# Optimization experiments

Hardware: AMD Instinct MI355X
Metric: run time of the kernel (lower is better)

Reference implementation:

```python
import jax, jax.numpy as jnp
import numpy as np

WS = 7
SHIFT = 3
NH = 16
DIM = 512
MLP = 2048
EMB = 512
EPS = 1e-6


def _rel_pos_index(ws):
    coords = np.stack(np.meshgrid(np.arange(ws), np.arange(ws), indexing='ij'))  # [2,ws,ws]
    flat = coords.reshape(2, -1)
    rel = flat[:, :, None] - flat[:, None, :]          # [2,N,N]
    rel = rel.transpose(1, 2, 0).copy()                # [N,N,2]
    rel[..., 0] += ws - 1
    rel[..., 1] += ws - 1
    rel[..., 0] *= 2 * ws - 1
    return rel.sum(-1)                                 # [N,N] int


def _shift_mask(H, W, ws, shift):
    img = np.zeros((H, W))
    cnt = 0
    for hs in (slice(0, -ws), slice(-ws, -shift), slice(-shift, None)):
        for wsl in (slice(0, -ws), slice(-ws, -shift), slice(-shift, None)):
            img[hs, wsl] = cnt
            cnt += 1
    win = img.reshape(H // ws, ws, W // ws, ws).transpose(0, 2, 1, 3).reshape(-1, ws * ws)
    diff = win[:, None, :] - win[:, :, None]           # [nW,N,N]
    return np.where(diff != 0, -100.0, 0.0).astype(np.float32)


def setup_inputs() -> dict:
    key = jax.random.key(0)
    ks = jax.random.split(key, 16)
    B, H, W = 16, 56, 56
    C, mlp, emb_dim = DIM, MLP, EMB
    std = 0.02
    inp = {
        'x': jax.random.normal(ks[0], (B, H * W, C), jnp.float32),
        'emb': jax.random.normal(ks[1], (B, emb_dim), jnp.float32),
        'adaLN_w': jax.random.normal(ks[2], (emb_dim, 6 * C), jnp.float32) * std,
        'adaLN_b': jnp.zeros((6 * C,), jnp.float32),
        'qkv_w': jax.random.normal(ks[3], (C, 3 * C), jnp.float32) * std,
        'qkv_b': jnp.zeros((3 * C,), jnp.float32),
        'proj_w': jax.random.normal(ks[4], (C, C), jnp.float32) * std,
        'proj_b': jnp.zeros((C,), jnp.float32),
        'rel_bias_table': jax.random.normal(ks[5], ((2 * WS - 1) ** 2, NH), jnp.float32) * std,
        'ff_w1': jax.random.normal(ks[6], (C, mlp), jnp.float32) * std,
        'ff_b1': jnp.zeros((mlp,), jnp.float32),
        'ff_w2': jax.random.normal(ks[7], (mlp, C), jnp.float32) * std,
        'ff_b2': jnp.zeros((C,), jnp.float32),
        'H': H,
        'W': W,
    }
    return inp


def _ln(t):
    mu = t.mean(-1, keepdims=True)
    var = ((t - mu) ** 2).mean(-1, keepdims=True)
    return (t - mu) / jnp.sqrt(var + EPS)


def reference(x, emb, adaLN_w, adaLN_b, qkv_w, qkv_b, proj_w, proj_b,
              rel_bias_table, ff_w1, ff_b1, ff_w2, ff_b2, H, W):
    B, L, C = x.shape
    dh = C // NH
    scale = dh ** (-0.5)
    N = WS * WS
    nWh, nWw = H // WS, W // WS
    nW = nWh * nWw

    # AdaLN modulation
    mod = jax.nn.silu(emb) @ adaLN_w + adaLN_b
    sh_sa, sc_sa, g_sa, sh_ff, sc_ff, g_ff = jnp.split(mod, 6, axis=-1)

    h = _ln(x) * (1.0 + sc_sa[:, None, :]) + sh_sa[:, None, :]
    h = h.reshape(B, H, W, C)
    h = jnp.roll(h, (-SHIFT, -SHIFT), axis=(1, 2))

    # window partition -> [B*nW, N, C]
    win = h.reshape(B, nWh, WS, nWw, WS, C).transpose(0, 1, 3, 2, 4, 5).reshape(B * nW, N, C)

    qkv = (win @ qkv_w + qkv_b).reshape(B * nW, N, 3, NH, dh).transpose(2, 0, 3, 1, 4)
    q, k, v = qkv[0], qkv[1], qkv[2]                   # [B_, NH, N, dh]
    attn = jnp.einsum('bhnd,bhmd->bhnm', q, k) * scale

    idx = _rel_pos_index(WS)
    bias = rel_bias_table[idx.reshape(-1)].reshape(N, N, NH).transpose(2, 0, 1)
    attn = attn + bias[None]

    mask = jnp.asarray(_shift_mask(H, W, WS, SHIFT))   # [nW,N,N]
    attn = attn.reshape(B, nW, NH, N, N) + mask[None, :, None]
    attn = jax.nn.softmax(attn.reshape(B * nW, NH, N, N), axis=-1)

    out = jnp.einsum('bhnm,bhmd->bnhd', attn, v).reshape(B * nW, N, C)
    out = out @ proj_w + proj_b

    # window reverse + unshift
    h = out.reshape(B, nWh, nWw, WS, WS, C).transpose(0, 1, 3, 2, 4, 5).reshape(B, H, W, C)
    h = jnp.roll(h, (SHIFT, SHIFT), axis=(1, 2)).reshape(B, L, C)

    x = x + g_sa[:, None, :] * h

    h = _ln(x) * (1.0 + sc_ff[:, None, :]) + sh_ff[:, None, :]
    ffo = jax.nn.gelu(h @ ff_w1 + ff_b1, approximate=False) @ ff_w2 + ff_b2
    return x + g_ff[:, None, :] * ffo
```

## Files before the change

kernel.cpp:

```cpp
#include <hip/hip_runtime.h>
#include <cmath>

typedef unsigned short u16;
typedef unsigned short u16x2 __attribute__((ext_vector_type(2)));
typedef unsigned short u16x4 __attribute__((ext_vector_type(4)));
typedef unsigned short u16x8 __attribute__((ext_vector_type(8)));
typedef short s16x8 __attribute__((ext_vector_type(8)));
typedef float f32x4 __attribute__((ext_vector_type(4)));
typedef float f32x2 __attribute__((ext_vector_type(2)));

#define B_SZ 16
#define HW 56
#define L_TOK 3136
#define C_DIM 512
#define NHEAD 16
#define DHEAD 32
#define WS7 7
#define NWIN 49
#define ROWS_TOTAL 50176
#define MLP_DIM 2048

__device__ __forceinline__ float bf2f(u16 u) {
    union { unsigned int i; float f; } z;
    z.i = ((unsigned int)u) << 16;
    return z.f;
}
__device__ __forceinline__ u16 f2bf(float f) {
    union { float f; unsigned int i; } z;
    z.f = f;
    unsigned int r = z.i + 0x7fffu + ((z.i >> 16) & 1u);
    return (u16)(r >> 16);
}

__device__ __forceinline__ void gl_lds16(const u16* g, u16* l) {
    __builtin_amdgcn_global_load_lds(
        (const __attribute__((address_space(1))) unsigned int*)g,
        (__attribute__((address_space(3))) unsigned int*)l,
        16, 0, 0);
}

__global__ __launch_bounds__(256)
void mod_kernel(const float* __restrict__ emb, const float* __restrict__ w,
                const float* __restrict__ bias, float* __restrict__ mod)
{
    int b = blockIdx.y;
    int o = blockIdx.x * 256 + threadIdx.x;
    __shared__ float se[512];
    for (int i = threadIdx.x; i < 512; i += 256) {
        float e = emb[b * 512 + i];
        se[i] = e / (1.0f + expf(-e));
    }
    __syncthreads();
    float acc = bias[o];
    #pragma unroll 8
    for (int k = 0; k < 512; ++k)
        acc += se[k] * w[(size_t)k * 3072 + o];
    mod[b * 3072 + o] = acc;
}

__global__ __launch_bounds__(1024)
void transpose_kernel(const float* __restrict__ W, u16* __restrict__ Wt, int K, int N)
{
    __shared__ float tile[32][33];
    int k0 = blockIdx.x * 32, n0 = blockIdx.y * 32;
    tile[threadIdx.y][threadIdx.x] = W[(size_t)(k0 + threadIdx.y) * N + (n0 + threadIdx.x)];
    __syncthreads();
    Wt[(size_t)(n0 + threadIdx.y) * K + (k0 + threadIdx.x)] = f2bf(tile[threadIdx.x][threadIdx.y]);
}

template<int WINDOWED>
__global__ __launch_bounds__(256)
void ln_kernel(const float* __restrict__ xin, const float* __restrict__ mod,
               u16* __restrict__ out, int shOff, int scOff, int rowBase)
{
    int wv   = threadIdx.x >> 6;
    int lane = threadIdx.x & 63;
    int rbl = blockIdx.x * 4 + wv;
    int rb  = rbl + rowBase;
    int b = rb / L_TOK, l = rb - b * L_TOK;
    const float* xr = xin + (size_t)rb * C_DIM;
    int c0 = lane * 8;
    f32x4 u0 = *(const f32x4*)(xr + c0);
    f32x4 u1 = *(const f32x4*)(xr + c0 + 4);
    float s = u0.x + u0.y + u0.z + u0.w + u1.x + u1.y + u1.z + u1.w;
    float q = u0.x*u0.x + u0.y*u0.y + u0.z*u0.z + u0.w*u0.w
            + u1.x*u1.x + u1.y*u1.y + u1.z*u1.z + u1.w*u1.w;
    #pragma unroll
    for (int off = 32; off > 0; off >>= 1) {
        s += __shfl_xor(s, off);
        q += __shfl_xor(q, off);
    }
    float mu = s * (1.0f / 512.0f);
    float var = q * (1.0f / 512.0f) - mu * mu;
    float rstd = rsqrtf(var + 1e-6f);
    const float* mb = mod + b * 3072;
    f32x4 sc0 = *(const f32x4*)(mb + scOff + c0);
    f32x4 sc1 = *(const f32x4*)(mb + scOff + c0 + 4);
    f32x4 sh0 = *(const f32x4*)(mb + shOff + c0);
    f32x4 sh1 = *(const f32x4*)(mb + shOff + c0 + 4);
    float y[8];
    y[0] = (u0.x - mu) * rstd * (1.0f + sc0.x) + sh0.x;
    y[1] = (u0.y - mu) * rstd * (1.0f + sc0.y) + sh0.y;
    y[2] = (u0.z - mu) * rstd * (1.0f + sc0.z) + sh0.z;
    y[3] = (u0.w - mu) * rstd * (1.0f + sc0.w) + sh0.w;
    y[4] = (u1.x - mu) * rstd * (1.0f + sc1.x) + sh1.x;
    y[5] = (u1.y - mu) * rstd * (1.0f + sc1.y) + sh1.y;
    y[6] = (u1.z - mu) * rstd * (1.0f + sc1.z) + sh1.z;
    y[7] = (u1.w - mu) * rstd * (1.0f + sc1.w) + sh1.w;
    size_t drow;
    if (WINDOWED) {
        int hh = l / HW, ww = l - hh * HW;
        int hs = hh - 3; if (hs < 0) hs += HW;
        int ws2 = ww - 3; if (ws2 < 0) ws2 += HW;
        int wi = (hs / WS7) * 8 + (ws2 / WS7);
        int n  = (hs % WS7) * WS7 + (ws2 % WS7);
        int b_local = rbl / L_TOK;
        drow = (size_t)((b_local * 64 + wi) * NWIN + n);
    } else {
        drow = (size_t)rbl;
    }
    u16x8 o;
    #pragma unroll
    for (int i = 0; i < 8; ++i) o[i] = f2bf(y[i]);
    *(u16x8*)(out + drow * C_DIM + c0) = o;
}

template<int EPI>
__global__ __launch_bounds__(256)
void gemm128(const u16* __restrict__ A, const u16* __restrict__ Bt,
             const float* __restrict__ bias, void* __restrict__ outv,
             const float* __restrict__ resid, const float* __restrict__ mod,
             int N, int K, int rowOffset)
{
    __shared__ u16 sA[128][32];
    __shared__ u16 sB[128][32];
    const int tid  = threadIdx.x;
    const int lane = tid & 63;
    const int wave = tid >> 6;
    const int wr = (wave >> 1) * 64;
    const int wc = (wave & 1) * 64;
    const int quad = lane >> 4;
    const int mrow = lane & 15;
    const int rowBase = blockIdx.x * 128;
    const int colBase = blockIdx.y * 128;

    const int r0   = wave * 32;
    const int lrow = lane >> 2;
    const int lcol = (lane & 3) * 8;
    const u16* gA = A  + (size_t)(rowBase + r0 + lrow) * K + lcol;
    const u16* gB = Bt + (size_t)(colBase + r0 + lrow) * K + lcol;
    u16* lA0 = &sA[r0][0];
    u16* lA1 = &sA[r0 + 16][0];
    u16* lB0 = &sB[r0][0];
    u16* lB1 = &sB[r0 + 16][0];
    const size_t gstep = (size_t)16 * K;

    f32x4 acc[4][4] = {};

    for (int kk = 0; kk < K; kk += 32) {
        __syncthreads();
        gl_lds16(gA + kk,         lA0);
        gl_lds16(gA + kk + gstep, lA1);
        gl_lds16(gB + kk,         lB0);
        gl_lds16(gB + kk + gstep, lB1);
        __syncthreads();
        s16x8 af[4], bg[4];
        #pragma unroll
        for (int tt = 0; tt < 4; ++tt) {
            af[tt] = *(const s16x8*)&sA[wr + tt * 16 + mrow][quad * 8];
            bg[tt] = *(const s16x8*)&sB[wc + tt * 16 + mrow][quad * 8];
        }
        #pragma unroll
        for (int tm = 0; tm < 4; ++tm)
            #pragma unroll
            for (int tn = 0; tn < 4; ++tn)
                acc[tm][tn] = __builtin_amdgcn_mfma_f32_16x16x32_bf16(
                    af[tm], bg[tn], acc[tm][tn], 0, 0, 0);
    }

    #pragma unroll
    for (int tm = 0; tm < 4; ++tm) {
        #pragma unroll
        for (int tn = 0; tn < 4; ++tn) {
            int col = colBase + wc + tn * 16 + mrow;
            float bv = bias[col];
            #pragma unroll
            for (int i = 0; i < 4; ++i) {
                int r = rowBase + wr + tm * 16 + quad * 4 + i;
                float v = acc[tm][tn][i] + bv;
                if constexpr (EPI == 0) {
                    ((u16*)outv)[(size_t)r * N + col] = f2bf(v);
                } else if constexpr (EPI == 1) {
                    float g = 0.5f * v * (1.0f + erff(v * 0.70710678118654752f));
                    ((u16*)outv)[(size_t)r * N + col] = f2bf(g);
                } else if constexpr (EPI == 2) {
                    int rg = r + rowOffset;
                    int b = rg / L_TOK;
                    int rem = rg - b * L_TOK;
                    int wi = rem / NWIN;
                    int n  = rem - wi * NWIN;
                    int hs  = (wi >> 3) * WS7 + n / WS7;
                    int ws2 = (wi & 7) * WS7 + n % WS7;
                    int hh = hs + 3;  if (hh >= HW)  hh -= HW;
                    int ww = ws2 + 3; if (ww >= HW)  ww -= HW;
                    size_t dst = ((size_t)(b * L_TOK + hh * HW + ww)) * C_DIM + col;
                    float g = mod[b * 3072 + 1024 + col];
                    ((float*)outv)[dst] = resid[dst] + g * v;
                } else {
                    int rg = r + rowOffset;
                    int b = rg / L_TOK;
                    size_t dst = (size_t)rg * C_DIM + col;
                    float g = mod[b * 3072 + 2560 + col];
                    ((float*)outv)[dst] = resid[dst] + g * v;
                }
            }
        }
    }
}

__global__ __launch_bounds__(256)
void attn_mfma(const u16* __restrict__ qkv, const float* __restrict__ bias_table,
               u16* __restrict__ out)
{
    const int w    = blockIdx.x;
    const int hg   = blockIdx.y;
    const int wave = threadIdx.x >> 6;
    const int lane = threadIdx.x & 63;
    const int h    = hg * 4 + wave;
    const int wi   = w & 63;
    const int quad = lane >> 4;
    const int mrow = lane & 15;

    __shared__ u16 sP[4][64][72];
    __shared__ u16 sVt[4][32][72];
    __shared__ float sBias[4][169];

    const u16* qb = qkv + (size_t)w * NWIN * 1536 + h * DHEAD;

    for (int e = lane; e < 169; e += 64)
        sBias[wave][e] = bias_table[e * NHEAD + h];

    #pragma unroll
    for (int rr = 0; rr < 4; ++rr) {
        int e = rr * 64 + lane;
        int r = e >> 2, d0 = (e & 3) * 8;
        u16x8 vv = {};
        if (e < 196)
            vv = *(const u16x8*)(qb + (size_t)r * 1536 + 1024 + d0);
        #pragma unroll
        for (int j = 0; j < 8; ++j)
            sVt[wave][d0 + j][r] = vv[j];
    }

    s16x8 qf[4], kf[4];
    #pragma unroll
    for (int t = 0; t < 4; ++t) {
        int r = t * 16 + mrow; if (r > 48) r = 48;
        qf[t] = *(const s16x8*)(qb + (size_t)r * 1536 + quad * 8);
        kf[t] = *(const s16x8*)(qb + (size_t)r * 1536 + 512 + quad * 8);
    }
    __syncthreads();

    f32x4 sacc[4][4] = {};
    #pragma unroll
    for (int tm = 0; tm < 4; ++tm)
        #pragma unroll
        for (int tn = 0; tn < 4; ++tn)
            sacc[tm][tn] = __builtin_amdgcn_mfma_f32_16x16x32_bf16(
                qf[tm], kf[tn], sacc[tm][tn], 0, 0, 0);

    const float scale = 0.17677669529663687f;
    const int wh = wi >> 3, ww = wi & 7;

    int khA[4], kwA[4], rkA[4], nOK[4];
    #pragma unroll
    for (int tn = 0; tn < 4; ++tn) {
        int n = tn * 16 + mrow;
        nOK[tn] = (n < NWIN);
        int nc = n > 48 ? 48 : n;
        khA[tn] = nc / 7; kwA[tn] = nc - khA[tn] * 7;
        int gkh = wh * 7 + khA[tn], gkw = ww * 7 + kwA[tn];
        rkA[tn] = (gkh < 49 ? 0 : (gkh < 53 ? 1 : 2)) * 3
                + (gkw < 49 ? 0 : (gkw < 53 ? 1 : 2));
    }

    #pragma unroll
    for (int tm = 0; tm < 4; ++tm) {
        #pragma unroll
        for (int i = 0; i < 4; ++i) {
            int m = tm * 16 + quad * 4 + i;
            int mc = m > 48 ? 48 : m;
            int qh = mc / 7, qw = mc - qh * 7;
            int gqh = wh * 7 + qh, gqw = ww * 7 + qw;
            int rq = (gqh < 49 ? 0 : (gqh < 53 ? 1 : 2)) * 3
                   + (gqw < 49 ? 0 : (gqw < 53 ? 1 : 2));
            float v[4];
            #pragma unroll
            for (int tn = 0; tn < 4; ++tn) {
                float s = sacc[tm][tn][i] * scale;
                s += sBias[wave][(qh - khA[tn] + 6) * 13 + (qw - kwA[tn] + 6)];
                if (rq != rkA[tn]) s -= 100.0f;
                v[tn] = nOK[tn] ? s : -1e30f;
            }
            float mx = fmaxf(fmaxf(v[0], v[1]), fmaxf(v[2], v[3]));
            mx = fmaxf(mx, __shfl_xor(mx, 1));
            mx = fmaxf(mx, __shfl_xor(mx, 2));
            mx = fmaxf(mx, __shfl_xor(mx, 4));
            mx = fmaxf(mx, __shfl_xor(mx, 8));
            float p0 = __expf(v[0] - mx), p1 = __expf(v[1] - mx);
            float p2 = __expf(v[2] - mx), p3 = __expf(v[3] - mx);
            float sum = p0 + p1 + p2 + p3;
            sum += __shfl_xor(sum, 1);
            sum += __shfl_xor(sum, 2);
            sum += __shfl_xor(sum, 4);
            sum += __shfl_xor(sum, 8);
            float inv = 1.0f / sum;
            float pp[4] = { p0 * inv, p1 * inv, p2 * inv, p3 * inv };
            #pragma unroll
            for (int tn = 0; tn < 4; ++tn) {
                float po = __shfl_xor(pp[tn], 1);
                if (!(mrow & 1)) {
                    unsigned int pk = (unsigned int)f2bf(pp[tn])
                                    | ((unsigned int)f2bf(po) << 16);
                    *(unsigned int*)&sP[wave][m][tn * 16 + mrow] = pk;
                }
            }
        }
    }
    __syncthreads();

    f32x4 oacc[2][4] = {};
    #pragma unroll
    for (int ks = 0; ks < 2; ++ks) {
        s16x8 vf[2], pf[4];
        #pragma unroll
        for (int td = 0; td < 2; ++td)
            vf[td] = *(const s16x8*)&sVt[wave][td * 16 + mrow][ks * 32 + quad * 8];
        #pragma unroll
        for (int tm = 0; tm < 4; ++tm)
            pf[tm] = *(const s16x8*)&sP[wave][tm * 16 + mrow][ks * 32 + quad * 8];
        #pragma unroll
        for (int td = 0; td < 2; ++td)
            #pragma unroll
            for (int tm = 0; tm < 4; ++tm)
                oacc[td][tm] = __builtin_amdgcn_mfma_f32_16x16x32_bf16(
                    vf[td], pf[tm], oacc[td][tm], 0, 0, 0);
    }

    #pragma unroll
    for (int tm = 0; tm < 4; ++tm) {
        int m = tm * 16 + mrow;
        if (m < NWIN) {
            u16* orow = out + ((size_t)(w * NWIN + m)) * C_DIM + h * DHEAD;
            #pragma unroll
            for (int td = 0; td < 2; ++td) {
                u16x4 ov;
                #pragma unroll
                for (int i = 0; i < 4; ++i) ov[i] = f2bf(oacc[td][tm][i]);
                *(u16x4*)(orow + td * 16 + quad * 4) = ov;
            }
        }
    }
}

extern "C" void kernel_launch(void* const* d_in, const int* in_sizes, int n_in,
                              void* d_out, int out_size, void* d_ws, size_t ws_size,
                              hipStream_t stream)
{
    const float* x       = (const float*)d_in[0];
    const float* emb     = (const float*)d_in[1];
    const float* adaLN_w = (const float*)d_in[2];
    const float* adaLN_b = (const float*)d_in[3];
    const float* qkv_w   = (const float*)d_in[4];
    const float* qkv_b   = (const float*)d_in[5];
    const float* proj_w  = (const float*)d_in[6];
    const float* proj_b  = (const float*)d_in[7];
    const float* relb    = (const float*)d_in[8];
    const float* ff_w1   = (const float*)d_in[9];
    const float* ff_b1   = (const float*)d_in[10];
    const float* ff_w2   = (const float*)d_in[11];
    const float* ff_b2   = (const float*)d_in[12];
    float* outp = (float*)d_out;

    char* ws = (char*)d_ws;
    float* mod   = (float*)(ws + 0);
    u16* wT_qkv  = (u16*)(ws + 196608);
    u16* wT_proj = (u16*)(ws + 1769472);
    u16* wT_ff1  = (u16*)(ws + 2293760);
    u16* wT_ff2  = (u16*)(ws + 4390912);
    char* slots  = ws + 6488064;

    const size_t perB_S = (size_t)L_TOK * C_DIM * sizeof(u16);
    const size_t perB_L = (size_t)L_TOK * MLP_DIM * sizeof(u16);

    int CB = 4;
    if (ws_size >= 6488064 + 8 * (perB_S + perB_L)) CB = 8;

    const int nChunks   = B_SZ / CB;
    const int chunkRows = CB * L_TOK;
    u16* slotS = (u16*)slots;
    u16* slotL = (u16*)(slots + (size_t)CB * perB_S);

    mod_kernel<<<dim3(12, 16), dim3(256), 0, stream>>>(emb, adaLN_w, adaLN_b, mod);
    transpose_kernel<<<dim3(16, 48), dim3(32, 32), 0, stream>>>(qkv_w,  wT_qkv, 512, 1536);
    transpose_kernel<<<dim3(16, 16), dim3(32, 32), 0, stream>>>(proj_w, wT_proj, 512, 512);
    transpose_kernel<<<dim3(16, 64), dim3(32, 32), 0, stream>>>(ff_w1,  wT_ff1, 512, 2048);
    transpose_kernel<<<dim3(64, 16), dim3(32, 32), 0, stream>>>(ff_w2,  wT_ff2, 2048, 512);

    for (int c = 0; c < nChunks; ++c) {
        int row0 = c * chunkRows;
        ln_kernel<1><<<dim3(chunkRows / 4), dim3(256), 0, stream>>>(
            x, mod, slotS, 0, 512, row0);
        gemm128<0><<<dim3(chunkRows / 128, 12), dim3(256), 0, stream>>>(
            slotS, wT_qkv, qkv_b, slotL, nullptr, mod, 1536, 512, 0);
        attn_mfma<<<dim3(CB * 64, 4), dim3(256), 0, stream>>>(slotL, relb, slotS);
        gemm128<2><<<dim3(chunkRows / 128, 4), dim3(256), 0, stream>>>(
            slotS, wT_proj, proj_b, outp, x, mod, 512, 512, row0);
        ln_kernel<0><<<dim3(chunkRows / 4), dim3(256), 0, stream>>>(
            outp, mod, slotS, 1536, 2048, row0);
        gemm128<1><<<dim3(chunkRows / 128, 16), dim3(256), 0, stream>>>(
            slotS, wT_ff1, ff_b1, slotL, nullptr, mod, 2048, 512, 0);
        gemm128<3><<<dim3(chunkRows / 128, 4), dim3(256), 0, stream>>>(
            slotL, wT_ff2, ff_b2, outp, outp, mod, 512, 2048, row0);
    }
}
```

Measured before the change: 1.091 ms.

## Triple-buffer LDS tiles in gemm128 to overlap global loads with MFMA

The GEMM main loop now keeps three LDS stages and issues the global-to-LDS copy for tile t+2 while tile t is computed. Explicit vmcnt waits and a single barrier per iteration replace the two syncthreads around each load. The goal is to hide global memory latency behind MFMA work. In exchange, LDS use per block triples, which can lower occupancy, and correctness depends on the hand-written waitcnt counts.

```diff
diff --git a/kernel.cpp b/kernel.cpp
--- a/kernel.cpp
+++ b/kernel.cpp
@@ -132,8 +132,8 @@
              const float* __restrict__ resid, const float* __restrict__ mod,
              int N, int K, int rowOffset)
 {
-    __shared__ u16 sA[128][32];
-    __shared__ u16 sB[128][32];
+    __shared__ u16 sA[3][128][32];
+    __shared__ u16 sB[3][128][32];
     const int tid  = threadIdx.x;
     const int lane = tid & 63;
     const int wave = tid >> 6;
@@ -149,26 +149,31 @@
     const int lcol = (lane & 3) * 8;
     const u16* gA = A  + (size_t)(rowBase + r0 + lrow) * K + lcol;
     const u16* gB = Bt + (size_t)(colBase + r0 + lrow) * K + lcol;
-    u16* lA0 = &sA[r0][0];
-    u16* lA1 = &sA[r0 + 16][0];
-    u16* lB0 = &sB[r0][0];
-    u16* lB1 = &sB[r0 + 16][0];
     const size_t gstep = (size_t)16 * K;
 
     f32x4 acc[4][4] = {};
-
-    for (int kk = 0; kk < K; kk += 32) {
-        __syncthreads();
-        gl_lds16(gA + kk,         lA0);
-        gl_lds16(gA + kk + gstep, lA1);
-        gl_lds16(gB + kk,         lB0);
-        gl_lds16(gB + kk + gstep, lB1);
-        __syncthreads();
+    const int nt = K >> 5;
+
+#define STAGE(bi, kk) do {                                 \
+    gl_lds16(gA + (kk),         &sA[bi][r0][0]);           \
+    gl_lds16(gA + (kk) + gstep, &sA[bi][r0 + 16][0]);      \
+    gl_lds16(gB + (kk),         &sB[bi][r0][0]);           \
+    gl_lds16(gB + (kk) + gstep, &sB[bi][r0 + 16][0]);      \
+} while (0)
+
+    STAGE(0, 0);
+    STAGE(1, 32);
+    asm volatile("s_waitcnt vmcnt(4)" ::: "memory");
+    __builtin_amdgcn_s_barrier();
+
+    int cur = 0, pre = 2;
+    for (int t = 0; t < nt; ++t) {
+        if (t + 2 < nt) STAGE(pre, (t + 2) * 32);
         s16x8 af[4], bg[4];
         #pragma unroll
         for (int tt = 0; tt < 4; ++tt) {
-            af[tt] = *(const s16x8*)&sA[wr + tt * 16 + mrow][quad * 8];
-            bg[tt] = *(const s16x8*)&sB[wc + tt * 16 + mrow][quad * 8];
+            af[tt] = *(const s16x8*)&sA[cur][wr + tt * 16 + mrow][quad * 8];
+            bg[tt] = *(const s16x8*)&sB[cur][wc + tt * 16 + mrow][quad * 8];
         }
         #pragma unroll
         for (int tm = 0; tm < 4; ++tm)
@@ -176,7 +181,17 @@
             for (int tn = 0; tn < 4; ++tn)
                 acc[tm][tn] = __builtin_amdgcn_mfma_f32_16x16x32_bf16(
                     af[tm], bg[tn], acc[tm][tn], 0, 0, 0);
-    }
+        if (t + 1 < nt) {
+            if (t + 2 < nt)
+                asm volatile("s_waitcnt vmcnt(4) lgkmcnt(0)" ::: "memory");
+            else
+                asm volatile("s_waitcnt vmcnt(0) lgkmcnt(0)" ::: "memory");
+            __builtin_amdgcn_s_barrier();
+        }
+        cur = (cur == 2) ? 0 : cur + 1;
+        pre = (pre == 2) ? 0 : pre + 1;
+    }
+#undef STAGE
 
     #pragma unroll
     for (int tm = 0; tm < 4; ++tm) {
```

New measurement: 1.159 ms. 6.2% more time.
